# Kernel optimization log

Hardware: AMD Instinct MI355X
Metric: run time of the kernel (lower is better)

Reference implementation:

```python
import jax, jax.numpy as jnp
import numpy as np

N = 50000      # nodes
E = 800000     # edges (before self loops)
NG = 512       # graphs in batch
D_IN = 128
D_H = 128
D_FC = 128
D_OUT = 2


def _gcn_conv(x, src, dst, norm, W, b, num_nodes):
    # x: [N, d_in] -> [N, d_out]; symmetric-normalized scatter-add over edges
    h = x @ W                              # [N, d_out]
    msg = h[src] * norm[:, None]           # [E+N, d_out]
    out = jax.ops.segment_sum(msg, dst, num_segments=num_nodes)
    return out + b


def setup_inputs() -> dict:
    key = jax.random.key(0)
    ks = jax.random.split(key, 12)
    x = jax.random.normal(ks[0], (N, D_IN), dtype=jnp.float32)
    edge_index = jax.random.randint(ks[1], (2, E), 0, N, dtype=jnp.int64)
    batch = jnp.sort(jax.random.randint(ks[2], (N,), 0, NG, dtype=jnp.int64))

    def glorot(k, shape):
        lim = float(np.sqrt(6.0 / (shape[0] + shape[1])))
        return jax.random.uniform(k, shape, jnp.float32, -lim, lim)

    return {
        "x": x, "edge_index": edge_index, "batch": batch,
        "W1": glorot(ks[3], (D_IN, D_H)), "b1": jnp.zeros((D_H,), jnp.float32),
        "W2": glorot(ks[4], (D_H, D_H)), "b2": jnp.zeros((D_H,), jnp.float32),
        "Wf1": glorot(ks[5], (D_H, D_FC)), "bf1": jnp.zeros((D_FC,), jnp.float32),
        "Wf2": glorot(ks[6], (D_FC, D_OUT)), "bf2": jnp.zeros((D_OUT,), jnp.float32),
    }


def reference(x, edge_index, batch, W1, b1, W2, b2, Wf1, bf1, Wf2, bf2):
    # add self loops (PyG GCNConv default)
    loops = jnp.arange(N, dtype=edge_index.dtype)
    src = jnp.concatenate([edge_index[0], loops])   # [E+N]
    dst = jnp.concatenate([edge_index[1], loops])   # [E+N]
    deg = jax.ops.segment_sum(jnp.ones_like(dst, dtype=x.dtype), dst, num_segments=N)
    dinv = jax.lax.rsqrt(deg)                       # deg >= 1 due to self loops
    norm = dinv[src] * dinv[dst]                    # [E+N]

    h = jax.nn.relu(_gcn_conv(x, src, dst, norm, W1, b1, N))
    h = jax.nn.relu(_gcn_conv(h, src, dst, norm, W2, b2, N))

    # global mean pool over graphs
    sums = jax.ops.segment_sum(h, batch, num_segments=NG)          # [NG, D_H]
    cnts = jax.ops.segment_sum(jnp.ones((N,), h.dtype), batch, num_segments=NG)
    g = sums / jnp.maximum(cnts, 1.0)[:, None]

    z = jax.nn.relu(g @ Wf1 + bf1)
    return z @ Wf2 + bf2
```

## Files before the change

### kernel.cpp

```cpp
#include <hip/hip_runtime.h>

typedef __attribute__((ext_vector_type(8))) short short8;
typedef __attribute__((ext_vector_type(4))) float f32x4;

__device__ __forceinline__ unsigned short f2b(float x) {
  unsigned u = __float_as_uint(x);
  u += 0x7FFF + ((u >> 16) & 1);
  return (unsigned short)(u >> 16);
}
__device__ __forceinline__ float b2f_lo(unsigned v) { return __uint_as_float(v << 16); }
__device__ __forceinline__ float b2f_hi(unsigned v) { return __uint_as_float(v & 0xFFFF0000u); }

#define EPB 4096
#define BKT 256
#define RPW 32

__global__ __launch_bounds__(256) void k_setup(
    const float* __restrict__ W1, unsigned short* __restrict__ Wt1,
    const float* __restrict__ W2, unsigned short* __restrict__ Wt2,
    const int* __restrict__ dst, int E, int nbuck, int* __restrict__ mat)
{
  __shared__ float tile[32][33];
  __shared__ int h[256];
  int t = threadIdx.x;
  if (blockIdx.x < 32) {
    const float* W = (blockIdx.x < 16) ? W1 : W2;
    unsigned short* Wt = (blockIdx.x < 16) ? Wt1 : Wt2;
    int bid = blockIdx.x & 15;
    int tx = t & 31, ty = t >> 5;
    int bx = bid & 3, by = bid >> 2;
    #pragma unroll
    for (int i = 0; i < 4; ++i)
      tile[ty + i * 8][tx] = W[(by * 32 + ty + i * 8) * 128 + bx * 32 + tx];
    __syncthreads();
    #pragma unroll
    for (int i = 0; i < 4; ++i)
      Wt[(bx * 32 + ty + i * 8) * 128 + by * 32 + tx] = f2b(tile[tx][ty + i * 8]);
  } else {
    int blk = blockIdx.x - 32;
    h[t] = 0;
    __syncthreads();
    int e0 = blk * EPB, e1 = min(e0 + EPB, E);
    for (int e = e0 + t; e < e1; e += 256) atomicAdd(&h[dst[e] >> 8], 1);
    __syncthreads();
    if (t < nbuck) mat[blk * nbuck + t] = h[t];
  }
}

__global__ __launch_bounds__(256) void k_excl(const int* __restrict__ mat, int neb, int nbuck,
                                              int* __restrict__ boff,
                                              int* __restrict__ rowptr, int N_) {
  __shared__ int s[256];
  int t = threadIdx.x;
  int sum = 0;
  if (t < nbuck) {
    #pragma unroll 8
    for (int r = 0; r < neb; ++r) sum += mat[r * nbuck + t];
  }
  s[t] = sum;
  __syncthreads();
  #pragma unroll
  for (int d = 1; d < 256; d <<= 1) {
    int u = (t >= d) ? s[t - d] : 0;
    __syncthreads();
    s[t] += u;
    __syncthreads();
  }
  if (t < nbuck) boff[t] = s[t] - sum;
  if (t == 0) { boff[nbuck] = s[255]; rowptr[N_] = s[255]; }
}

__global__ __launch_bounds__(256) void k_colscan(int* __restrict__ mat, int neb, int nbuck,
                                                 const int* __restrict__ boff,
                                                 float* __restrict__ sums,
                                                 int* __restrict__ cnt, int ng) {
  __shared__ int s[256];
  int b = blockIdx.x, t = threadIdx.x;
  int v = (t < neb) ? mat[t * nbuck + b] : 0;
  s[t] = v;
  __syncthreads();
  #pragma unroll
  for (int d = 1; d < 256; d <<= 1) {
    int u = (t >= d) ? s[t - d] : 0;
    __syncthreads();
    s[t] += u;
    __syncthreads();
  }
  if (t < neb) mat[t * nbuck + b] = boff[b] + s[t] - v;
  int tot_e = ng * 128;
  for (int i = b * 256 + t; i < tot_e; i += gridDim.x * 256) sums[i] = 0.f;
  for (int i = b * 256 + t; i < ng; i += gridDim.x * 256) cnt[i] = 0;
}

__global__ __launch_bounds__(256) void k_part(const int* __restrict__ src,
                                              const int* __restrict__ dst, int E, int nbuck,
                                              const int* __restrict__ mat,
                                              unsigned* __restrict__ staged) {
  __shared__ int cur[256];
  int t = threadIdx.x;
  if (t < nbuck) cur[t] = mat[blockIdx.x * nbuck + t];
  __syncthreads();
  int e0 = blockIdx.x * EPB, e1 = min(e0 + EPB, E);
  for (int e = e0 + t; e < e1; e += 256) {
    int d = dst[e];
    int pos = atomicAdd(&cur[d >> 8], 1);
    staged[pos] = ((unsigned)(d & 255) << 16) | (unsigned)src[e];
  }
}

__global__ __launch_bounds__(256) void k_csr(const unsigned* __restrict__ staged,
                                             const int* __restrict__ boff, int N_,
                                             float* __restrict__ dinv, int* __restrict__ rowptr,
                                             unsigned short* __restrict__ csr16) {
  __shared__ int cnt[256];
  __shared__ int cur[256];
  int b = blockIdx.x, t = threadIdx.x;
  int lo = boff[b], hi = boff[b + 1];
  cnt[t] = 0;
  __syncthreads();
  for (int i = lo + t; i < hi; i += 256) atomicAdd(&cnt[staged[i] >> 16], 1);
  __syncthreads();
  int v = cnt[t];
  #pragma unroll
  for (int d = 1; d < 256; d <<= 1) {
    int u = (t >= d) ? cnt[t - d] : 0;
    __syncthreads();
    cnt[t] += u;
    __syncthreads();
  }
  int start = lo + cnt[t] - v;
  cur[t] = start;
  int node = (b << 8) + t;
  if (node < N_) {
    rowptr[node] = start;
    dinv[node] = rsqrtf((float)(v + 1));
  }
  __syncthreads();
  for (int i = lo + t; i < hi; i += 256) {
    unsigned e = staged[i];
    int pos = atomicAdd(&cur[e >> 16], 1);
    csr16[pos] = (unsigned short)(e & 0xFFFFu);
  }
}

template<int A_F32>
__global__ __launch_bounds__(256) void k_mfma_gemm(
    const void* __restrict__ Ap, const unsigned short* __restrict__ Wt,
    const float* __restrict__ dinv, unsigned short* __restrict__ Out, int M)
{
  int wv = threadIdx.x >> 6, lane = threadIdx.x & 63;
  int r0 = blockIdx.x * 64 + wv * 16;
  if (r0 >= M) return;
  int arow = r0 + (lane & 15);
  int kb = (lane >> 4) * 8;
  short8 a[4];
  if (A_F32) {
    const float* Ar = (const float*)Ap + (size_t)arow * 128 + kb;
    #pragma unroll
    for (int ks = 0; ks < 4; ++ks) {
      float4 u = *(const float4*)(Ar + ks * 32);
      float4 v = *(const float4*)(Ar + ks * 32 + 4);
      short8 tt;
      tt[0] = (short)f2b(u.x); tt[1] = (short)f2b(u.y);
      tt[2] = (short)f2b(u.z); tt[3] = (short)f2b(u.w);
      tt[4] = (short)f2b(v.x); tt[5] = (short)f2b(v.y);
      tt[6] = (short)f2b(v.z); tt[7] = (short)f2b(v.w);
      a[ks] = tt;
    }
  } else {
    const unsigned short* Ar = (const unsigned short*)Ap + (size_t)arow * 128 + kb;
    #pragma unroll
    for (int ks = 0; ks < 4; ++ks)
      a[ks] = *(const short8*)(Ar + ks * 32);
  }
  f32x4 acc[8];
  #pragma unroll
  for (int i = 0; i < 8; ++i) acc[i] = (f32x4){0.f, 0.f, 0.f, 0.f};
  const unsigned short* Bc = Wt + (size_t)(lane & 15) * 128 + kb;
  #pragma unroll
  for (int ct = 0; ct < 8; ++ct) {
    const unsigned short* B = Bc + ct * 16 * 128;
    #pragma unroll
    for (int ks = 0; ks < 4; ++ks)
      acc[ct] = __builtin_amdgcn_mfma_f32_16x16x32_bf16(
          a[ks], *(const short8*)(B + ks * 32), acc[ct], 0, 0, 0);
  }
  int orow = r0 + (lane >> 4) * 4;
  int ocol = lane & 15;
  float s0 = dinv[orow], s1 = dinv[orow + 1], s2 = dinv[orow + 2], s3 = dinv[orow + 3];
  #pragma unroll
  for (int ct = 0; ct < 8; ++ct) {
    unsigned short* o = Out + (size_t)orow * 128 + ct * 16 + ocol;
    o[0]   = f2b(acc[ct][0] * s0);
    o[128] = f2b(acc[ct][1] * s1);
    o[256] = f2b(acc[ct][2] * s2);
    o[384] = f2b(acc[ct][3] * s3);
  }
}

__global__ __launch_bounds__(256) void k_gather_post(
    const unsigned short* __restrict__ csr16, const int* __restrict__ rowptr,
    const unsigned short* __restrict__ P, const float* __restrict__ dinv,
    const float* __restrict__ bias, unsigned short* __restrict__ R, int n)
{
  int node = blockIdx.x * 8 + (threadIdx.x >> 5);
  if (node >= n) return;
  int lane = threadIdx.x & 31;
  int lo = rowptr[node], hi = rowptr[node + 1];
  float a0 = 0.f, a1 = 0.f, a2 = 0.f, a3 = 0.f;
  int e = lo;
  for (; e + 4 <= hi; e += 4) {
    int s0 = csr16[e], s1 = csr16[e + 1], s2 = csr16[e + 2], s3 = csr16[e + 3];
    uint2 v0 = ((const uint2*)(P + (size_t)s0 * 128))[lane];
    uint2 v1 = ((const uint2*)(P + (size_t)s1 * 128))[lane];
    uint2 v2 = ((const uint2*)(P + (size_t)s2 * 128))[lane];
    uint2 v3 = ((const uint2*)(P + (size_t)s3 * 128))[lane];
    a0 += b2f_lo(v0.x) + b2f_lo(v1.x) + b2f_lo(v2.x) + b2f_lo(v3.x);
    a1 += b2f_hi(v0.x) + b2f_hi(v1.x) + b2f_hi(v2.x) + b2f_hi(v3.x);
    a2 += b2f_lo(v0.y) + b2f_lo(v1.y) + b2f_lo(v2.y) + b2f_lo(v3.y);
    a3 += b2f_hi(v0.y) + b2f_hi(v1.y) + b2f_hi(v2.y) + b2f_hi(v3.y);
  }
  for (; e < hi; ++e) {
    int s = csr16[e];
    uint2 v = ((const uint2*)(P + (size_t)s * 128))[lane];
    a0 += b2f_lo(v.x); a1 += b2f_hi(v.x);
    a2 += b2f_lo(v.y); a3 += b2f_hi(v.y);
  }
  float dv = dinv[node];
  uint2 hv = ((const uint2*)(P + (size_t)node * 128))[lane];
  float4 bb = ((const float4*)bias)[lane];
  float r0 = fmaxf(dv * (a0 + b2f_lo(hv.x)) + bb.x, 0.f);
  float r1 = fmaxf(dv * (a1 + b2f_hi(hv.x)) + bb.y, 0.f);
  float r2 = fmaxf(dv * (a2 + b2f_lo(hv.y)) + bb.z, 0.f);
  float r3 = fmaxf(dv * (a3 + b2f_hi(hv.y)) + bb.w, 0.f);
  uint2 pack;
  pack.x = (unsigned)f2b(r0) | ((unsigned)f2b(r1) << 16);
  pack.y = (unsigned)f2b(r2) | ((unsigned)f2b(r3) << 16);
  ((uint2*)(R + (size_t)node * 128))[lane] = pack;
}

__global__ __launch_bounds__(256) void k_pool_sum(
    const unsigned short* __restrict__ h2, const int* __restrict__ batch, int n,
    float* __restrict__ sums, int* __restrict__ cnt)
{
  int wid = blockIdx.x * 4 + (threadIdx.x >> 6);
  int lane = threadIdx.x & 63;
  int r0 = wid * RPW;
  if (r0 >= n) return;
  int r1 = min(r0 + RPW, n);
  const unsigned* H = (const unsigned*)h2;
  int gcur = batch[r0];
  float ax = 0.f, ay = 0.f;
  int run = 0;
  for (int r = r0; r < r1; ++r) {
    int g = batch[r];
    if (g != gcur) {
      atomicAdd(&sums[(size_t)gcur * 128 + 2 * lane], ax);
      atomicAdd(&sums[(size_t)gcur * 128 + 2 * lane + 1], ay);
      if (lane == 0) atomicAdd(&cnt[gcur], run);
      ax = ay = 0.f; run = 0; gcur = g;
    }
    unsigned v = H[(size_t)r * 64 + lane];
    ax += b2f_lo(v); ay += b2f_hi(v); ++run;
  }
  atomicAdd(&sums[(size_t)gcur * 128 + 2 * lane], ax);
  atomicAdd(&sums[(size_t)gcur * 128 + 2 * lane + 1], ay);
  if (lane == 0) atomicAdd(&cnt[gcur], run);
}

__global__ __launch_bounds__(128) void k_fc(
    const float* __restrict__ sums, const int* __restrict__ cnt,
    const float* __restrict__ Wf1, const float* __restrict__ bf1,
    const float* __restrict__ Wf2, const float* __restrict__ bf2,
    float* __restrict__ out)
{
  __shared__ float gl[128];
  __shared__ float red0[128];
  __shared__ float red1[128];
  int g = blockIdx.x, t = threadIdx.x;
  float c = (float)cnt[g];
  gl[t] = sums[(size_t)g * 128 + t] / fmaxf(c, 1.f);
  __syncthreads();
  float z0 = 0.f, z1 = 0.f, z2 = 0.f, z3 = 0.f;
  #pragma unroll
  for (int k = 0; k < 32; ++k) {
    z0 += gl[k]      * Wf1[k * 128 + t];
    z1 += gl[k + 32] * Wf1[(k + 32) * 128 + t];
    z2 += gl[k + 64] * Wf1[(k + 64) * 128 + t];
    z3 += gl[k + 96] * Wf1[(k + 96) * 128 + t];
  }
  float z = fmaxf((z0 + z1) + (z2 + z3) + bf1[t], 0.f);
  red0[t] = z * Wf2[2 * t];
  red1[t] = z * Wf2[2 * t + 1];
  __syncthreads();
  #pragma unroll
  for (int d = 64; d > 0; d >>= 1) {
    if (t < d) { red0[t] += red0[t + d]; red1[t] += red1[t + d]; }
    __syncthreads();
  }
  if (t == 0) {
    out[g * 2]     = red0[0] + bf2[0];
    out[g * 2 + 1] = red1[0] + bf2[1];
  }
}

extern "C" void kernel_launch(void* const* d_in, const int* in_sizes, int n_in,
                              void* d_out, int out_size, void* d_ws, size_t ws_size,
                              hipStream_t stream) {
  const float* x    = (const float*)d_in[0];
  const int*   ei   = (const int*)d_in[1];
  const int*   batch= (const int*)d_in[2];
  const float* W1   = (const float*)d_in[3];
  const float* b1   = (const float*)d_in[4];
  const float* W2   = (const float*)d_in[5];
  const float* b2   = (const float*)d_in[6];
  const float* Wf1  = (const float*)d_in[7];
  const float* bf1  = (const float*)d_in[8];
  const float* Wf2  = (const float*)d_in[9];
  const float* bf2  = (const float*)d_in[10];
  float* out = (float*)d_out;

  const int N  = in_sizes[0] / 128;
  const int E  = in_sizes[1] / 2;
  const int NG = out_size / 2;
  const int* srcp = ei;
  const int* dstp = ei + E;

  const int nbuck = (N + BKT - 1) / BKT;
  const int neb   = (E + EPB - 1) / EPB;

  char* ws = (char*)d_ws;
  size_t off = 0;
  auto carve = [&](size_t bytes) { void* p = ws + off; off += (bytes + 255) & ~(size_t)255; return p; };
  float* dinv   = (float*)carve((size_t)N * 4);
  int*   rowptr = (int*)  carve((size_t)(N + 1) * 4);
  int*   boff   = (int*)  carve((size_t)(nbuck + 1) * 4);
  int*   mat    = (int*)  carve((size_t)neb * nbuck * 4);
  unsigned*       staged = (unsigned*)      carve((size_t)E * 4);
  unsigned short* csr16  = (unsigned short*)carve((size_t)E * 2);
  unsigned short* Wt1 = (unsigned short*)carve(128 * 128 * 2);
  unsigned short* Wt2 = (unsigned short*)carve(128 * 128 * 2);
  float* sums   = (float*)carve((size_t)NG * 128 * 4);
  int*   cntg   = (int*)  carve((size_t)NG * 4);
  const size_t nb_row = (size_t)N * 128 * 2;
  unsigned short* U0 = (unsigned short*)carve(nb_row);
  unsigned short* U1 = (unsigned short*)carve(nb_row);

  k_setup<<<32 + neb, 256, 0, stream>>>(W1, Wt1, W2, Wt2, dstp, E, nbuck, mat);
  k_excl   <<<1, 256, 0, stream>>>(mat, neb, nbuck, boff, rowptr, N);
  k_colscan<<<nbuck, 256, 0, stream>>>(mat, neb, nbuck, boff, sums, cntg, NG);
  k_part<<<neb, 256, 0, stream>>>(srcp, dstp, E, nbuck, mat, staged);
  k_csr <<<nbuck, 256, 0, stream>>>(staged, boff, N, dinv, rowptr, csr16);

  const int gblocks = (N + 63) / 64;
  k_mfma_gemm<1><<<gblocks, 256, 0, stream>>>(x, Wt1, dinv, U0, N);
  k_gather_post<<<(N + 7) / 8, 256, 0, stream>>>(csr16, rowptr, U0, dinv, b1, U1, N);
  k_mfma_gemm<0><<<gblocks, 256, 0, stream>>>(U1, Wt2, dinv, U0, N);
  k_gather_post<<<(N + 7) / 8, 256, 0, stream>>>(csr16, rowptr, U0, dinv, b2, U1, N);

  const int pblocks = (N + RPW * 4 - 1) / (RPW * 4);
  k_pool_sum<<<pblocks, 256, 0, stream>>>(U1, batch, N, sums, cntg);
  k_fc<<<NG, 128, 0, stream>>>(sums, cntg, Wf1, bf1, Wf2, bf2, out);
}
```

Measured before the change: 177.3 us.

## Drop column-scan kernel via atomic bucket cursors, reuse GEMM B-fragments, unroll gather

Removes the k_colscan kernel. Each partition block now claims its slot range per bucket with a global atomicAdd on a cursor array, and the zeroing of pool sums moves into k_part. The MFMA GEMM keeps all B fragments in registers and processes two 16-row tiles per wave, so weight loads are amortised and fewer blocks are launched. The gather loop gains an 8-wide unroll to put more loads in flight. The price is a non-deterministic edge order within each bucket and higher register pressure in the GEMM.

```diff
diff --git a/kernel.cpp b/kernel.cpp
--- a/kernel.cpp
+++ b/kernel.cpp
@@ -48,7 +48,7 @@
 }
 
 __global__ __launch_bounds__(256) void k_excl(const int* __restrict__ mat, int neb, int nbuck,
-                                              int* __restrict__ boff,
+                                              int* __restrict__ boff, int* __restrict__ cursor,
                                               int* __restrict__ rowptr, int N_) {
   __shared__ int s[256];
   int t = threadIdx.x;
@@ -66,39 +66,23 @@
     s[t] += u;
     __syncthreads();
   }
-  if (t < nbuck) boff[t] = s[t] - sum;
+  if (t < nbuck) { boff[t] = s[t] - sum; cursor[t] = s[t] - sum; }
   if (t == 0) { boff[nbuck] = s[255]; rowptr[N_] = s[255]; }
-}
-
-__global__ __launch_bounds__(256) void k_colscan(int* __restrict__ mat, int neb, int nbuck,
-                                                 const int* __restrict__ boff,
-                                                 float* __restrict__ sums,
-                                                 int* __restrict__ cnt, int ng) {
-  __shared__ int s[256];
-  int b = blockIdx.x, t = threadIdx.x;
-  int v = (t < neb) ? mat[t * nbuck + b] : 0;
-  s[t] = v;
-  __syncthreads();
-  #pragma unroll
-  for (int d = 1; d < 256; d <<= 1) {
-    int u = (t >= d) ? s[t - d] : 0;
-    __syncthreads();
-    s[t] += u;
-    __syncthreads();
-  }
-  if (t < neb) mat[t * nbuck + b] = boff[b] + s[t] - v;
-  int tot_e = ng * 128;
-  for (int i = b * 256 + t; i < tot_e; i += gridDim.x * 256) sums[i] = 0.f;
-  for (int i = b * 256 + t; i < ng; i += gridDim.x * 256) cnt[i] = 0;
 }
 
 __global__ __launch_bounds__(256) void k_part(const int* __restrict__ src,
                                               const int* __restrict__ dst, int E, int nbuck,
                                               const int* __restrict__ mat,
-                                              unsigned* __restrict__ staged) {
+                                              int* __restrict__ cursor,
+                                              unsigned* __restrict__ staged,
+                                              float* __restrict__ sums,
+                                              int* __restrict__ cnt, int ng) {
   __shared__ int cur[256];
   int t = threadIdx.x;
-  if (t < nbuck) cur[t] = mat[blockIdx.x * nbuck + t];
+  if (t < nbuck) {
+    int c = mat[blockIdx.x * nbuck + t];
+    cur[t] = c ? atomicAdd(&cursor[t], c) : 0;
+  }
   __syncthreads();
   int e0 = blockIdx.x * EPB, e1 = min(e0 + EPB, E);
   for (int e = e0 + t; e < e1; e += 256) {
@@ -106,6 +90,9 @@
     int pos = atomicAdd(&cur[d >> 8], 1);
     staged[pos] = ((unsigned)(d & 255) << 16) | (unsigned)src[e];
   }
+  int tot_e = ng * 128;
+  for (int i = blockIdx.x * 256 + t; i < tot_e; i += gridDim.x * 256) sums[i] = 0.f;
+  for (int i = blockIdx.x * 256 + t; i < ng; i += gridDim.x * 256) cnt[i] = 0;
 }
 
 __global__ __launch_bounds__(256) void k_csr(const unsigned* __restrict__ staged,
@@ -149,52 +136,60 @@
     const float* __restrict__ dinv, unsigned short* __restrict__ Out, int M)
 {
   int wv = threadIdx.x >> 6, lane = threadIdx.x & 63;
-  int r0 = blockIdx.x * 64 + wv * 16;
-  if (r0 >= M) return;
-  int arow = r0 + (lane & 15);
   int kb = (lane >> 4) * 8;
-  short8 a[4];
-  if (A_F32) {
-    const float* Ar = (const float*)Ap + (size_t)arow * 128 + kb;
-    #pragma unroll
-    for (int ks = 0; ks < 4; ++ks) {
-      float4 u = *(const float4*)(Ar + ks * 32);
-      float4 v = *(const float4*)(Ar + ks * 32 + 4);
-      short8 tt;
-      tt[0] = (short)f2b(u.x); tt[1] = (short)f2b(u.y);
-      tt[2] = (short)f2b(u.z); tt[3] = (short)f2b(u.w);
-      tt[4] = (short)f2b(v.x); tt[5] = (short)f2b(v.y);
-      tt[6] = (short)f2b(v.z); tt[7] = (short)f2b(v.w);
-      a[ks] = tt;
+  short8 bf[8][4];
+  const unsigned short* Bc = Wt + (size_t)(lane & 15) * 128 + kb;
+  #pragma unroll
+  for (int ct = 0; ct < 8; ++ct)
+    #pragma unroll
+    for (int ks = 0; ks < 4; ++ks)
+      bf[ct][ks] = *(const short8*)(Bc + ct * 16 * 128 + ks * 32);
+
+  int r0 = (blockIdx.x * 4 + wv) * 32;
+  #pragma unroll
+  for (int rt = 0; rt < 2; ++rt) {
+    int rbase = r0 + rt * 16;
+    if (rbase >= M) return;
+    int arow = rbase + (lane & 15);
+    short8 a[4];
+    if (A_F32) {
+      const float* Ar = (const float*)Ap + (size_t)arow * 128 + kb;
+      #pragma unroll
+      for (int ks = 0; ks < 4; ++ks) {
+        float4 u = *(const float4*)(Ar + ks * 32);
+        float4 v = *(const float4*)(Ar + ks * 32 + 4);
+        short8 tt;
+        tt[0] = (short)f2b(u.x); tt[1] = (short)f2b(u.y);
+        tt[2] = (short)f2b(u.z); tt[3] = (short)f2b(u.w);
+        tt[4] = (short)f2b(v.x); tt[5] = (short)f2b(v.y);
+        tt[6] = (short)f2b(v.z); tt[7] = (short)f2b(v.w);
+        a[ks] = tt;
+      }
+    } else {
+      const unsigned short* Ar = (const unsigned short*)Ap + (size_t)arow * 128 + kb;
+      #pragma unroll
+      for (int ks = 0; ks < 4; ++ks)
+        a[ks] = *(const short8*)(Ar + ks * 32);
     }
-  } else {
-    const unsigned short* Ar = (const unsigned short*)Ap + (size_t)arow * 128 + kb;
-    #pragma unroll
-    for (int ks = 0; ks < 4; ++ks)
-      a[ks] = *(const short8*)(Ar + ks * 32);
-  }
-  f32x4 acc[8];
-  #pragma unroll
-  for (int i = 0; i < 8; ++i) acc[i] = (f32x4){0.f, 0.f, 0.f, 0.f};
-  const unsigned short* Bc = Wt + (size_t)(lane & 15) * 128 + kb;
-  #pragma unroll
-  for (int ct = 0; ct < 8; ++ct) {
-    const unsigned short* B = Bc + ct * 16 * 128;
-    #pragma unroll
-    for (int ks = 0; ks < 4; ++ks)
-      acc[ct] = __builtin_amdgcn_mfma_f32_16x16x32_bf16(
-          a[ks], *(const short8*)(B + ks * 32), acc[ct], 0, 0, 0);
-  }
-  int orow = r0 + (lane >> 4) * 4;
-  int ocol = lane & 15;
-  float s0 = dinv[orow], s1 = dinv[orow + 1], s2 = dinv[orow + 2], s3 = dinv[orow + 3];
-  #pragma unroll
-  for (int ct = 0; ct < 8; ++ct) {
-    unsigned short* o = Out + (size_t)orow * 128 + ct * 16 + ocol;
-    o[0]   = f2b(acc[ct][0] * s0);
-    o[128] = f2b(acc[ct][1] * s1);
-    o[256] = f2b(acc[ct][2] * s2);
-    o[384] = f2b(acc[ct][3] * s3);
+    f32x4 acc[8];
+    #pragma unroll
+    for (int i = 0; i < 8; ++i) acc[i] = (f32x4){0.f, 0.f, 0.f, 0.f};
+    #pragma unroll
+    for (int ct = 0; ct < 8; ++ct)
+      #pragma unroll
+      for (int ks = 0; ks < 4; ++ks)
+        acc[ct] = __builtin_amdgcn_mfma_f32_16x16x32_bf16(a[ks], bf[ct][ks], acc[ct], 0, 0, 0);
+    int orow = rbase + (lane >> 4) * 4;
+    int ocol = lane & 15;
+    float s0 = dinv[orow], s1 = dinv[orow + 1], s2 = dinv[orow + 2], s3 = dinv[orow + 3];
+    #pragma unroll
+    for (int ct = 0; ct < 8; ++ct) {
+      unsigned short* o = Out + (size_t)orow * 128 + ct * 16 + ocol;
+      o[0]   = f2b(acc[ct][0] * s0);
+      o[128] = f2b(acc[ct][1] * s1);
+      o[256] = f2b(acc[ct][2] * s2);
+      o[384] = f2b(acc[ct][3] * s3);
+    }
   }
 }
 
@@ -209,6 +204,26 @@
   int lo = rowptr[node], hi = rowptr[node + 1];
   float a0 = 0.f, a1 = 0.f, a2 = 0.f, a3 = 0.f;
   int e = lo;
+  for (; e + 8 <= hi; e += 8) {
+    int s0 = csr16[e],     s1 = csr16[e + 1], s2 = csr16[e + 2], s3 = csr16[e + 3];
+    int s4 = csr16[e + 4], s5 = csr16[e + 5], s6 = csr16[e + 6], s7 = csr16[e + 7];
+    uint2 v0 = ((const uint2*)(P + (size_t)s0 * 128))[lane];
+    uint2 v1 = ((const uint2*)(P + (size_t)s1 * 128))[lane];
+    uint2 v2 = ((const uint2*)(P + (size_t)s2 * 128))[lane];
+    uint2 v3 = ((const uint2*)(P + (size_t)s3 * 128))[lane];
+    uint2 v4 = ((const uint2*)(P + (size_t)s4 * 128))[lane];
+    uint2 v5 = ((const uint2*)(P + (size_t)s5 * 128))[lane];
+    uint2 v6 = ((const uint2*)(P + (size_t)s6 * 128))[lane];
+    uint2 v7 = ((const uint2*)(P + (size_t)s7 * 128))[lane];
+    a0 += b2f_lo(v0.x) + b2f_lo(v1.x) + b2f_lo(v2.x) + b2f_lo(v3.x)
+        + b2f_lo(v4.x) + b2f_lo(v5.x) + b2f_lo(v6.x) + b2f_lo(v7.x);
+    a1 += b2f_hi(v0.x) + b2f_hi(v1.x) + b2f_hi(v2.x) + b2f_hi(v3.x)
+        + b2f_hi(v4.x) + b2f_hi(v5.x) + b2f_hi(v6.x) + b2f_hi(v7.x);
+    a2 += b2f_lo(v0.y) + b2f_lo(v1.y) + b2f_lo(v2.y) + b2f_lo(v3.y)
+        + b2f_lo(v4.y) + b2f_lo(v5.y) + b2f_lo(v6.y) + b2f_lo(v7.y);
+    a3 += b2f_hi(v0.y) + b2f_hi(v1.y) + b2f_hi(v2.y) + b2f_hi(v3.y)
+        + b2f_hi(v4.y) + b2f_hi(v5.y) + b2f_hi(v6.y) + b2f_hi(v7.y);
+  }
   for (; e + 4 <= hi; e += 4) {
     int s0 = csr16[e], s1 = csr16[e + 1], s2 = csr16[e + 2], s3 = csr16[e + 3];
     uint2 v0 = ((const uint2*)(P + (size_t)s0 * 128))[lane];
@@ -335,6 +350,7 @@
   float* dinv   = (float*)carve((size_t)N * 4);
   int*   rowptr = (int*)  carve((size_t)(N + 1) * 4);
   int*   boff   = (int*)  carve((size_t)(nbuck + 1) * 4);
+  int*   cursor = (int*)  carve((size_t)256 * 4);
   int*   mat    = (int*)  carve((size_t)neb * nbuck * 4);
   unsigned*       staged = (unsigned*)      carve((size_t)E * 4);
   unsigned short* csr16  = (unsigned short*)carve((size_t)E * 2);
@@ -347,12 +363,11 @@
   unsigned short* U1 = (unsigned short*)carve(nb_row);
 
   k_setup<<<32 + neb, 256, 0, stream>>>(W1, Wt1, W2, Wt2, dstp, E, nbuck, mat);
-  k_excl   <<<1, 256, 0, stream>>>(mat, neb, nbuck, boff, rowptr, N);
-  k_colscan<<<nbuck, 256, 0, stream>>>(mat, neb, nbuck, boff, sums, cntg, NG);
-  k_part<<<neb, 256, 0, stream>>>(srcp, dstp, E, nbuck, mat, staged);
+  k_excl<<<1, 256, 0, stream>>>(mat, neb, nbuck, boff, cursor, rowptr, N);
+  k_part<<<neb, 256, 0, stream>>>(srcp, dstp, E, nbuck, mat, cursor, staged, sums, cntg, NG);
   k_csr <<<nbuck, 256, 0, stream>>>(staged, boff, N, dinv, rowptr, csr16);
 
-  const int gblocks = (N + 63) / 64;
+  const int gblocks = (N + 127) / 128;
   k_mfma_gemm<1><<<gblocks, 256, 0, stream>>>(x, Wt1, dinv, U0, N);
   k_gather_post<<<(N + 7) / 8, 256, 0, stream>>>(csr16, rowptr, U0, dinv, b1, U1, N);
   k_mfma_gemm<0><<<gblocks, 256, 0, stream>>>(U1, Wt2, dinv, U0, N);
```

Result: faster. 160.9 us (-9.3%).
